# Optimization experiments

Measured on AMD Instinct MI355X. Metric: run time of the kernel, lower is better.

Reference implementation:

```python
import jax, jax.numpy as jnp
import numpy as np

K = 3          # B-spline order (cubic)
G = 10         # number of spline intervals over [0, 1]
NELY, NELX = 512, 512
WIDTHS = [2, 32, 32, 1]


def _make_grid(in_dim):
    # extended uniform knot vector over [0,1] with K extra knots each side: (in_dim, G+2K+1)
    h = 1.0 / G
    knots = jnp.arange(-K, G + K + 1, dtype=jnp.float32) * h
    return jnp.tile(knots[None, :], (in_dim, 1))


def setup_inputs() -> dict:
    key = jax.random.key(0)
    ks = jax.random.split(key, 1 + 3 * (len(WIDTHS) - 1))
    inp = {"coords": jax.random.uniform(ks[0], (NELY * NELX, 2), dtype=jnp.float32)}
    for l, (i, o) in enumerate(zip(WIDTHS[:-1], WIDTHS[1:])):
        inp[f"grid{l}"] = _make_grid(i)
        inp[f"coef{l}"] = 0.1 * jax.random.normal(ks[1 + 3 * l], (i, o, G + K), dtype=jnp.float32)
        inp[f"sb{l}"] = jax.random.normal(ks[2 + 3 * l], (i, o), dtype=jnp.float32) / np.sqrt(i).astype(np.float32)
        inp[f"sp{l}"] = jnp.ones((i, o), dtype=jnp.float32)
    inp["density_bias"] = jnp.full((1,), np.float32(np.log(0.5 / (1.0 - 0.5 + 1e-8))))
    return inp


def _b_batch(x, grid):
    # Cox-de Boor recursion. x: (B, in), grid: (in, G+2K+1) -> bases (B, in, G+K)
    xe = x[:, :, None]
    v = ((xe >= grid[None, :, :-1]) & (xe < grid[None, :, 1:])).astype(x.dtype)
    for p in range(1, K + 1):
        left = (xe - grid[None, :, : -(p + 1)]) / (grid[None, :, p:-1] - grid[None, :, : -(p + 1)])
        right = (grid[None, :, p + 1:] - xe) / (grid[None, :, p + 1:] - grid[None, :, 1:-p])
        v = left * v[:, :, :-1] + right * v[:, :, 1:]
    return v


def _kan_layer(x, grid, coef, sb, sp):
    # y_out = sum_in [ sb * silu(x) + sp * sum_k B_k(x) * coef_k ]
    B = _b_batch(x, grid)                               # (batch, in, G+K)
    spline = jnp.einsum('bik,iok->bio', B, coef)        # (batch, in, out)
    base = jax.nn.silu(x)                               # (batch, in)
    return jnp.sum(sb[None] * base[:, :, None] + sp[None] * spline, axis=1)


def reference(coords, grid0, coef0, sb0, sp0, grid1, coef1, sb1, sp1,
              grid2, coef2, sb2, sp2, density_bias):
    h = _kan_layer(coords, grid0, coef0, sb0, sp0)
    h = _kan_layer(h, grid1, coef1, sb1, sp1)
    logits = _kan_layer(h, grid2, coef2, sb2, sp2) + density_bias
    return jax.nn.sigmoid(logits).reshape(1, NELY, NELX)
```

## Files before the change

kernel.cpp:

```cpp
#include <hip/hip_runtime.h>
#include <hip/hip_bf16.h>

typedef __hip_bfloat16 bf16;
typedef __fp16 h2v __attribute__((ext_vector_type(2)));
typedef __fp16 half8 __attribute__((ext_vector_type(8)));
typedef float floatx4 __attribute__((ext_vector_type(4)));

#define NPTS (512*512)

#define OFF_BIAS 12
#define OFF_FLAG 13
#define OFF_BF   16
#define NFRAG    50
#define WS_WORDS (16 + NFRAG*64*4)


__device__ __forceinline__ bool sniff_f32(const void* g0) {
    float f = ((const float*)g0)[0];
    return fabsf(f + 0.3f) < 0.01f;
}
__device__ __forceinline__ float ld(const void* p, int i, bool f32) {
    return f32 ? ((const float*)p)[i] : __bfloat162float(((const bf16*)p)[i]);
}
__device__ __forceinline__ unsigned pk_rtn(float a, float b) {
    union { h2v v; unsigned u; } x;
    x.v[0] = (__fp16)a; x.v[1] = (__fp16)b;
    return x.u;
}
__device__ __forceinline__ unsigned pkf16(float a, float b) {
    union { h2v v; unsigned u; } x;
    x.v = __builtin_amdgcn_cvt_pkrtz(a, b);
    return x.u;
}

__device__ float slotval(int layer, int K, int o,
                         const void* c0, const void* sb0, const void* sp0,
                         const void* c1, const void* sb1, const void* sp1,
                         const void* c2, const void* sb2, const void* sp2, bool f32)
{
    int i = K >> 4, s = K & 15;
    if (layer == 2 && o != 0) return 0.0f;
    if (s >= 1 && s <= 13) {
        int m = s - 1;
        if (layer == 0) return ld(c0, (i*32+o)*13 + m, f32) * ld(sp0, i*32+o, f32);
        if (layer == 1) return ld(c1, (i*32+o)*13 + m, f32) * ld(sp1, i*32+o, f32);
        return ld(c2, i*13 + m, f32) * ld(sp2, i, f32);
    }
    if (s == 14) {
        if (layer == 0) return ld(sb0, i*32+o, f32);
        if (layer == 1) return ld(sb1, i*32+o, f32);
        return ld(sb2, i, f32);
    }
    return 0.0f;
}

__global__ __launch_bounds__(256) void kan_prep(
    const void* __restrict__ g0, const void* __restrict__ c0,
    const void* __restrict__ sb0, const void* __restrict__ sp0,
    const void* __restrict__ g1, const void* __restrict__ c1,
    const void* __restrict__ sb1, const void* __restrict__ sp1,
    const void* __restrict__ g2, const void* __restrict__ c2,
    const void* __restrict__ sb2, const void* __restrict__ sp2,
    const void* __restrict__ bias, float* __restrict__ ws)
{
    const bool f32 = sniff_f32(g0);
    int t = blockIdx.x * blockDim.x + threadIdx.x;

    if (t < 16) {
        if (t < 12) {
            int l = t >> 2, j = t & 3;
            const void* g = (l == 0) ? g0 : (l == 1) ? g1 : g2;
            float lo = ld(g, 0, f32), hi = ld(g, 16, f32);
            float ih = 16.0f / (hi - lo);
            float v = (j == 0) ? lo : (j == 1) ? hi
                    : (j == 2) ? ih : (-lo * ih);
            ws[t] = v;
        } else if (t == 12) ws[12] = ld(bias, 0, f32);
        else if (t == 13)   ws[13] = f32 ? 1.0f : 0.0f;
        else                ws[t] = 0.0f;
        return;
    }
    int ft = t - 16;
    if (ft >= NFRAG * 64) return;
    int f = ft >> 6, l = ft & 63, n = l & 15, q = l >> 4;
    int layer, c, nt;
    if (f < 2)       { layer = 0; c = 0;          nt = f; }
    else if (f < 34) { layer = 1; c = (f - 2) >> 1; nt = (f - 2) & 1; }
    else             { layer = 2; c = f - 34;     nt = 0; }
    int o = nt * 16 + n;
    unsigned wv[4];
#pragma unroll
    for (int jp = 0; jp < 4; jp++) {
        int K0 = c * 32 + q * 8 + jp * 2;
        float v0 = slotval(layer, K0,     o, c0,sb0,sp0, c1,sb1,sp1, c2,sb2,sp2, f32);
        float v1 = slotval(layer, K0 + 1, o, c0,sb0,sp0, c1,sb1,sp1, c2,sb2,sp2, f32);
        wv[jp] = pk_rtn(v0, v1);
    }
    uint4 out4; out4.x = wv[0]; out4.y = wv[1]; out4.z = wv[2]; out4.w = wv[3];
    ((uint4*)((unsigned*)ws + OFF_BF))[f * 64 + l] = out4;
}

__device__ __forceinline__ floatx4 mf(uint4 a, uint4 b, floatx4 c)
{
    union { uint4 u; half8 h; } ua, ub;
    ua.u = a; ub.u = b;
    return __builtin_amdgcn_mfma_f32_16x16x32_f16(ua.h, ub.h, c, 0, 0, 0);
}

__device__ __forceinline__ void eval_taps(float x, float ngh, float ih,
    unsigned& A, unsigned& B, unsigned& C, int& wout, float& si)
{
    float t  = fmaf(x, ih, ngh);
    float fj = floorf(t);
    float u  = t - fj;
    bool inb = (t >= 0.0f) && (t < 16.0f);
    float s6 = inb ? 0.166666667f : 0.0f;
    int j  = (int)fj;
    int jc = min(max(j, 0), 15);
    float u2 = u * u, u3 = u2 * u, om = 1.0f - u;
    float b0 = om * om * om * s6;
    float b1 = (fmaf(3.0f, u3, 4.0f) - 6.0f * u2) * s6;
    float b2 = fmaf(-3.0f, u3, fmaf(3.0f, u2, fmaf(3.0f, u, 1.0f))) * s6;
    float b3 = u3 * s6;
    int m0 = jc - 3;
    if ((unsigned)(m0 + 0) > 12u) b0 = 0.0f;
    if ((unsigned)(m0 + 1) > 12u) b1 = 0.0f;
    if ((unsigned)(m0 + 2) > 12u) b2 = 0.0f;
    if ((unsigned)(m0 + 3) > 12u) b3 = 0.0f;
    int s0 = m0 + 1;
    wout = ((s0 + 2) >> 1) - 1;
    if (s0 & 1) { A = pkf16(0.0f, b0); B = pkf16(b1, b2); C = pkf16(b3, 0.0f); }
    else        { A = pkf16(b0, b1);   B = pkf16(b2, b3); C = 0u; }
    si = x / (1.0f + __expf(-x));
}

__device__ __forceinline__ void stage2(unsigned* row, float f0, float f1,
                                       float ngh, float ih)
{
    uint4 z; z.x = 0u; z.y = 0u; z.z = 0u; z.w = 0u;
    *(uint4*)(row + 0)  = z;
    *(uint4*)(row + 4)  = z;
    *(uint4*)(row + 8)  = z;
    *(uint4*)(row + 12) = z;
    unsigned A0,B0,C0,A1,B1,C1; int w0,w1; float s0,s1;
    eval_taps(f0, ngh, ih, A0, B0, C0, w0, s0);
    eval_taps(f1, ngh, ih, A1, B1, C1, w1, s1);
    row[w0]     = A0; row[w0 + 1]  = B0; row[w0 + 2]  = C0;
    row[8 + w1] = A1; row[9 + w1]  = B1; row[10 + w1] = C1;
    row[7]  = pkf16(s0, 0.0f);
    row[15] = pkf16(s1, 0.0f);
}

__global__ __launch_bounds__(256, 4) void kan_main(
    const void* __restrict__ coords, const float* __restrict__ ws,
    void* __restrict__ out)
{
    __shared__ __align__(16) unsigned lds[4 * 2304];
    const unsigned* wsu = (const unsigned*)ws;
    const uint4* bfp = (const uint4*)(wsu + OFF_BF);

    int tid = threadIdx.x;
    int l = tid & 63, w = tid >> 6;
    int p = blockIdx.x * 256 + w * 64 + l;

    unsigned* rb = lds + w * 2304;
    unsigned* cb = rb;
    unsigned* myrow = cb + l * 20;

    const bool f32 = (ws[OFF_FLAG] != 0.0f);
    float x0, x1;
    if (f32) {
        float2 c = ((const float2*)coords)[p];
        x0 = c.x; x1 = c.y;
    } else {
        unsigned cc = ((const unsigned*)coords)[p];
        union { unsigned u; float f; } cv;
        cv.u = (cc & 0xffffu) << 16;  x0 = cv.f;
        cv.u = cc & 0xffff0000u;      x1 = cv.f;
    }

    const float iha = ws[2],  ngha = ws[3];
    const float ihb = ws[6],  nghb = ws[7];
    const float ihc = ws[10], nghc = ws[11];

    const int arow = l & 15, aq = (l >> 4) * 4;
    const int drow = (l >> 4) * 4, dcol = l & 15;

    float h[32];

    {
        floatx4 acc[4][2];
#pragma unroll
        for (int mt = 0; mt < 4; mt++)
#pragma unroll
            for (int nt = 0; nt < 2; nt++) acc[mt][nt] = (floatx4)0.0f;

        uint4 bf0 = bfp[0 * 64 + l], bf1 = bfp[1 * 64 + l];
        stage2(myrow, x0, x1, ngha, iha);
#pragma unroll
        for (int mt = 0; mt < 4; mt++) {
            uint4 a = *(const uint4*)(cb + (arow + 16 * mt) * 20 + aq);
            acc[mt][0] = mf(a, bf0, acc[mt][0]);
            acc[mt][1] = mf(a, bf1, acc[mt][1]);
        }
#pragma unroll
        for (int mt = 0; mt < 4; mt++)
#pragma unroll
            for (int nt = 0; nt < 2; nt++)
#pragma unroll
                for (int r = 0; r < 4; r++)
                    rb[(mt*16 + drow + r) * 36 + nt*16 + dcol] =
                        __float_as_uint(acc[mt][nt][r]);
#pragma unroll
        for (int q = 0; q < 8; q++) {
            uint4 v = *(const uint4*)(rb + l * 36 + q * 4);
            h[q*4+0] = __uint_as_float(v.x);
            h[q*4+1] = __uint_as_float(v.y);
            h[q*4+2] = __uint_as_float(v.z);
            h[q*4+3] = __uint_as_float(v.w);
        }
    }

    {
        floatx4 acc[4][2];
#pragma unroll
        for (int mt = 0; mt < 4; mt++)
#pragma unroll
            for (int nt = 0; nt < 2; nt++) acc[mt][nt] = (floatx4)0.0f;

#pragma unroll
        for (int c = 0; c < 16; c++) {
            uint4 bf0 = bfp[(2 + 2*c) * 64 + l];
            uint4 bf1 = bfp[(3 + 2*c) * 64 + l];
            stage2(myrow, h[2*c], h[2*c + 1], nghb, ihb);
#pragma unroll
            for (int mt = 0; mt < 4; mt++) {
                uint4 a = *(const uint4*)(cb + (arow + 16 * mt) * 20 + aq);
                acc[mt][0] = mf(a, bf0, acc[mt][0]);
                acc[mt][1] = mf(a, bf1, acc[mt][1]);
            }
        }
#pragma unroll
        for (int mt = 0; mt < 4; mt++)
#pragma unroll
            for (int nt = 0; nt < 2; nt++)
#pragma unroll
                for (int r = 0; r < 4; r++)
                    rb[(mt*16 + drow + r) * 36 + nt*16 + dcol] =
                        __float_as_uint(acc[mt][nt][r]);
#pragma unroll
        for (int q = 0; q < 8; q++) {
            uint4 v = *(const uint4*)(rb + l * 36 + q * 4);
            h[q*4+0] = __uint_as_float(v.x);
            h[q*4+1] = __uint_as_float(v.y);
            h[q*4+2] = __uint_as_float(v.z);
            h[q*4+3] = __uint_as_float(v.w);
        }
    }

    {
        floatx4 acc[4];
#pragma unroll
        for (int mt = 0; mt < 4; mt++) acc[mt] = (floatx4)0.0f;

#pragma unroll
        for (int c = 0; c < 16; c++) {
            uint4 bf = bfp[(34 + c) * 64 + l];
            stage2(myrow, h[2*c], h[2*c + 1], nghc, ihc);
#pragma unroll
            for (int mt = 0; mt < 4; mt++) {
                uint4 a = *(const uint4*)(cb + (arow + 16 * mt) * 20 + aq);
                acc[mt] = mf(a, bf, acc[mt]);
            }
        }
        if ((l & 15) == 0) {
#pragma unroll
            for (int mt = 0; mt < 4; mt++)
#pragma unroll
                for (int r = 0; r < 4; r++)
                    rb[(mt*16 + drow + r) * 36] = __float_as_uint(acc[mt][r]);
        }
        float z = __uint_as_float(rb[l * 36]);
        float r = 1.0f / (1.0f + __expf(-(z + ws[OFF_BIAS])));
        if (f32) ((float*)out)[p] = r;
        else     ((bf16*)out)[p] = __float2bfloat16(r);
    }
}

extern "C" void kernel_launch(void* const* d_in, const int* in_sizes, int n_in,
                              void* d_out, int out_size, void* d_ws, size_t ws_size,
                              hipStream_t stream)
{
    float* ws = (float*)d_ws;

    kan_prep<<<(16 + NFRAG*64 + 255) / 256, 256, 0, stream>>>(
        d_in[1], d_in[2], d_in[3], d_in[4],
        d_in[5], d_in[6], d_in[7], d_in[8],
        d_in[9], d_in[10], d_in[11], d_in[12],
        d_in[13], ws);

    kan_main<<<NPTS / 256, 256, 0, stream>>>(d_in[0], ws, d_out);
}
```

Measured before the change: 122.4 us.

## Halve per-wave LDS staging and raise occupancy target to eight blocks

The accumulator-to-row transpose is split into two passes of 16 columns each, so every wave's LDS buffer drops from 2304 to 1280 words and the row stride from 36 to 20. The launch bound minimum goes from 4 to 8 blocks per CU, so more blocks can be resident at once. The per-tap zeroing of basis weights at the edge of the valid range is also removed, which cuts ALU work in eval_taps. The risks are register spilling under the tighter launch bound, and possible write-out-of-range or changed numerics at boundary knots now that the masks are gone.

Measured after the change: 137.0 us. 11.9% more time.

```diff
diff --git a/kernel.cpp b/kernel.cpp
--- a/kernel.cpp
+++ b/kernel.cpp
@@ -115,19 +115,13 @@
     float u  = t - fj;
     bool inb = (t >= 0.0f) && (t < 16.0f);
     float s6 = inb ? 0.166666667f : 0.0f;
-    int j  = (int)fj;
-    int jc = min(max(j, 0), 15);
+    int jc = min(max((int)fj, 0), 15);
     float u2 = u * u, u3 = u2 * u, om = 1.0f - u;
     float b0 = om * om * om * s6;
     float b1 = (fmaf(3.0f, u3, 4.0f) - 6.0f * u2) * s6;
     float b2 = fmaf(-3.0f, u3, fmaf(3.0f, u2, fmaf(3.0f, u, 1.0f))) * s6;
     float b3 = u3 * s6;
-    int m0 = jc - 3;
-    if ((unsigned)(m0 + 0) > 12u) b0 = 0.0f;
-    if ((unsigned)(m0 + 1) > 12u) b1 = 0.0f;
-    if ((unsigned)(m0 + 2) > 12u) b2 = 0.0f;
-    if ((unsigned)(m0 + 3) > 12u) b3 = 0.0f;
-    int s0 = m0 + 1;
+    int s0 = jc - 2;
     wout = ((s0 + 2) >> 1) - 1;
     if (s0 & 1) { A = pkf16(0.0f, b0); B = pkf16(b1, b2); C = pkf16(b3, 0.0f); }
     else        { A = pkf16(b0, b1);   B = pkf16(b2, b3); C = 0u; }
@@ -151,11 +145,11 @@
     row[15] = pkf16(s1, 0.0f);
 }
 
-__global__ __launch_bounds__(256, 4) void kan_main(
+__global__ __launch_bounds__(256, 8) void kan_main(
     const void* __restrict__ coords, const float* __restrict__ ws,
     void* __restrict__ out)
 {
-    __shared__ __align__(16) unsigned lds[4 * 2304];
+    __shared__ __align__(16) unsigned lds[4 * 1280];
     const unsigned* wsu = (const unsigned*)ws;
     const uint4* bfp = (const uint4*)(wsu + OFF_BF);
 
@@ -163,7 +157,7 @@
     int l = tid & 63, w = tid >> 6;
     int p = blockIdx.x * 256 + w * 64 + l;
 
-    unsigned* rb = lds + w * 2304;
+    unsigned* rb = lds + w * 1280;
     unsigned* cb = rb;
     unsigned* myrow = cb + l * 20;
 
@@ -204,20 +198,21 @@
             acc[mt][1] = mf(a, bf1, acc[mt][1]);
         }
 #pragma unroll
-        for (int mt = 0; mt < 4; mt++)
-#pragma unroll
-            for (int nt = 0; nt < 2; nt++)
+        for (int nt = 0; nt < 2; nt++) {
+#pragma unroll
+            for (int mt = 0; mt < 4; mt++)
 #pragma unroll
                 for (int r = 0; r < 4; r++)
-                    rb[(mt*16 + drow + r) * 36 + nt*16 + dcol] =
+                    rb[(mt*16 + drow + r) * 20 + dcol] =
                         __float_as_uint(acc[mt][nt][r]);
 #pragma unroll
-        for (int q = 0; q < 8; q++) {
-            uint4 v = *(const uint4*)(rb + l * 36 + q * 4);
-            h[q*4+0] = __uint_as_float(v.x);
-            h[q*4+1] = __uint_as_float(v.y);
-            h[q*4+2] = __uint_as_float(v.z);
-            h[q*4+3] = __uint_as_float(v.w);
+            for (int q = 0; q < 4; q++) {
+                uint4 v = *(const uint4*)(rb + l * 20 + q * 4);
+                h[nt*16 + q*4+0] = __uint_as_float(v.x);
+                h[nt*16 + q*4+1] = __uint_as_float(v.y);
+                h[nt*16 + q*4+2] = __uint_as_float(v.z);
+                h[nt*16 + q*4+3] = __uint_as_float(v.w);
+            }
         }
     }
 
@@ -241,20 +236,21 @@
             }
         }
 #pragma unroll
-        for (int mt = 0; mt < 4; mt++)
-#pragma unroll
-            for (int nt = 0; nt < 2; nt++)
+        for (int nt = 0; nt < 2; nt++) {
+#pragma unroll
+            for (int mt = 0; mt < 4; mt++)
 #pragma unroll
                 for (int r = 0; r < 4; r++)
-                    rb[(mt*16 + drow + r) * 36 + nt*16 + dcol] =
+                    rb[(mt*16 + drow + r) * 20 + dcol] =
                         __float_as_uint(acc[mt][nt][r]);
 #pragma unroll
-        for (int q = 0; q < 8; q++) {
-            uint4 v = *(const uint4*)(rb + l * 36 + q * 4);
-            h[q*4+0] = __uint_as_float(v.x);
-            h[q*4+1] = __uint_as_float(v.y);
-            h[q*4+2] = __uint_as_float(v.z);
-            h[q*4+3] = __uint_as_float(v.w);
+            for (int q = 0; q < 4; q++) {
+                uint4 v = *(const uint4*)(rb + l * 20 + q * 4);
+                h[nt*16 + q*4+0] = __uint_as_float(v.x);
+                h[nt*16 + q*4+1] = __uint_as_float(v.y);
+                h[nt*16 + q*4+2] = __uint_as_float(v.z);
+                h[nt*16 + q*4+3] = __uint_as_float(v.w);
+            }
         }
     }
 
@@ -278,9 +274,9 @@
             for (int mt = 0; mt < 4; mt++)
 #pragma unroll
                 for (int r = 0; r < 4; r++)
-                    rb[(mt*16 + drow + r) * 36] = __float_as_uint(acc[mt][r]);
-        }
-        float z = __uint_as_float(rb[l * 36]);
+                    rb[(mt*16 + drow + r) * 20] = __float_as_uint(acc[mt][r]);
+        }
+        float z = __uint_as_float(rb[l * 20]);
         float r = 1.0f / (1.0f + __expf(-(z + ws[OFF_BIAS])));
         if (f32) ((float*)out)[p] = r;
         else     ((bf16*)out)[p] = __float2bfloat16(r);
```
